# Kernel optimization log

Hardware: AMD Instinct MI355X
Metric: run time of the kernel (lower is better)

## Reference

```python
import jax, jax.numpy as jnp
import numpy as np
from jax import lax

B, T_ENC, T_DEC, H, L, F, NC, S = 1024, 128, 64, 128, 2, 16, 4, 8
X_DIM = 2
IN_DIM = X_DIM + F          # encoder GRU input_size = 18
H_ENC = 2 * H               # encoder hidden = 256 (mean/logvar)
H_DEC = H + NC              # decoder hidden = 132 (concat_cond_ts=False)


def _gru_params(key, in_dim, hid):
    k1, k2, k3, k4 = jax.random.split(key, 4)
    s = 1.0 / np.sqrt(hid)
    u = lambda k, shp: jax.random.uniform(k, shp, minval=-s, maxval=s, dtype=jnp.float32)
    return u(k1, (3 * hid, in_dim)), u(k2, (3 * hid, hid)), u(k3, (3 * hid,)), u(k4, (3 * hid,))


def gru_cell(x, h, Wih, Whh, bih, bhh):
    # torch GRU cell: r,z,n gate ordering
    gi = x @ Wih.T + bih
    gh = h @ Whh.T + bhh
    hd = h.shape[-1]
    ir, iz, inn = gi[:, :hd], gi[:, hd:2 * hd], gi[:, 2 * hd:]
    hr, hz, hn = gh[:, :hd], gh[:, hd:2 * hd], gh[:, 2 * hd:]
    r = jax.nn.sigmoid(ir + hr)
    zg = jax.nn.sigmoid(iz + hz)
    n = jnp.tanh(inn + r * hn)
    return (1.0 - zg) * n + zg * h


def setup_inputs() -> dict:
    key = jax.random.key(0)
    ks = jax.random.split(key, 12)
    x = jax.random.normal(ks[0], (B, T_ENC, X_DIM), dtype=jnp.float32)
    features = jax.random.normal(ks[1], (B, T_ENC + T_DEC, F), dtype=jnp.float32)
    lengths = jax.random.randint(ks[2], (B,), T_ENC // 2, T_ENC + 1)
    mask = (jnp.arange(T_ENC)[None, :] < lengths[:, None]).astype(jnp.int32)
    eps = jax.random.normal(ks[3], (S, L, B, H), dtype=jnp.float32)
    enc0 = _gru_params(ks[4], IN_DIM, H_ENC)
    enc1 = _gru_params(ks[5], H_ENC, H_ENC)
    dec0 = _gru_params(ks[6], 2, H_DEC)
    dec1 = _gru_params(ks[7], H_DEC, H_DEC)
    sm = 1.0 / np.sqrt(H)
    W1 = jax.random.uniform(ks[8], (H // 2, H), minval=-sm, maxval=sm, dtype=jnp.float32)
    b1 = jax.random.uniform(ks[9], (H // 2,), minval=-sm, maxval=sm, dtype=jnp.float32)
    s2 = 1.0 / np.sqrt(H // 2)
    W2 = jax.random.uniform(ks[10], (2, H // 2), minval=-s2, maxval=s2, dtype=jnp.float32)
    b2 = jax.random.uniform(ks[11], (2,), minval=-s2, maxval=s2, dtype=jnp.float32)
    return dict(
        x=x, features=features, mask=mask, eps=eps,
        nsteps_encode=T_ENC, nsteps_decode=T_DEC, n_elbo_samp=S,
        enc_Wih0=enc0[0], enc_Whh0=enc0[1], enc_bih0=enc0[2], enc_bhh0=enc0[3],
        enc_Wih1=enc1[0], enc_Whh1=enc1[1], enc_bih1=enc1[2], enc_bhh1=enc1[3],
        dec_Wih0=dec0[0], dec_Whh0=dec0[1], dec_bih0=dec0[2], dec_bhh0=dec0[3],
        dec_Wih1=dec1[0], dec_Whh1=dec1[1], dec_bih1=dec1[2], dec_bhh1=dec1[3],
        W1=W1, b1=b1, W2=W2, b2=b2,
    )


def reference(x, features, mask, eps, nsteps_encode, nsteps_decode, n_elbo_samp,
              enc_Wih0, enc_Whh0, enc_bih0, enc_bhh0,
              enc_Wih1, enc_Whh1, enc_bih1, enc_bhh1,
              dec_Wih0, dec_Whh0, dec_bih0, dec_bhh0,
              dec_Wih1, dec_Whh1, dec_bih1, dec_bhh1,
              W1, b1, W2, b2):
    n_hidden = W1.shape[1]
    batch = x.shape[0]
    enc_input = jnp.concatenate([x, features[:, :nsteps_encode, :]], axis=-1)
    m = mask.astype(bool)

    def mlp(h):
        return jax.nn.softplus(jax.nn.relu(h @ W1.T + b1) @ W2.T + b2)

    # --- encoder: 2-layer GRU with pack_padded semantics (freeze h / zero out past length) ---
    def enc_step(h, xm):
        xt, mt = xm
        h0n = gru_cell(xt, h[0], enc_Wih0, enc_Whh0, enc_bih0, enc_bhh0)
        h0n = jnp.where(mt[:, None], h0n, h[0])
        h1n = gru_cell(h0n, h[1], enc_Wih1, enc_Whh1, enc_bih1, enc_bhh1)
        h1n = jnp.where(mt[:, None], h1n, h[1])
        out = jnp.where(mt[:, None], h1n, 0.0)
        return jnp.stack([h0n, h1n]), out

    h_init = jnp.zeros((2, batch, enc_Whh0.shape[1]), dtype=x.dtype)
    hT, outs = lax.scan(enc_step, h_init, (enc_input.transpose(1, 0, 2), m.T))
    enc_out = outs.transpose(1, 0, 2)                 # [B, T_enc, 2H]
    enc_pred = mlp(enc_out[..., :n_hidden])           # [B, T_enc, 2]
    z_mean = hT[:, :, :n_hidden]                      # [L, B, H]
    z_logvar = hT[:, :, n_hidden:]

    last = enc_pred[:, -1, :]                         # [B, 2]
    feat_cond = features[:, nsteps_encode, :4]        # cond_inds = [0,1,2,3]

    # --- decoder: sequential single-step GRU, h0 = cat(z, cond feats) ---
    def decode_one(e):
        z = e * jnp.exp(0.5 * z_logvar) + z_mean      # [L, B, H]
        fc = jnp.broadcast_to(feat_cond[None], (z.shape[0],) + feat_cond.shape)
        h0 = jnp.concatenate([z, fc], axis=-1)        # [L, B, H+NC]
        def step(carry, _):
            inp, h = carry
            d0 = gru_cell(inp, h[0], dec_Wih0, dec_Whh0, dec_bih0, dec_bhh0)
            d1 = gru_cell(d0, h[1], dec_Wih1, dec_Whh1, dec_bih1, dec_bhh1)
            out = mlp(d1[:, :n_hidden])
            return (out, jnp.stack([d0, d1])), out
        _, outs_d = lax.scan(step, (last, h0), None, length=nsteps_decode - 1)
        return jnp.concatenate([last[None], outs_d], axis=0)   # [T_dec, B, 2]

    dec = jax.vmap(decode_one)(eps)                   # [S, T_dec, B, 2]
    dec_preds = dec.transpose(0, 2, 1, 3)             # [S, B, T_dec, 2]
    enc_stack = jnp.broadcast_to(enc_pred[None, :, :-1, :],
                                 (n_elbo_samp, batch, enc_pred.shape[1] - 1, 2))
    return enc_stack, dec_preds
```

## Files before the change

kernel.cpp:

```cpp
#include <hip/hip_runtime.h>
#include <hip/hip_bf16.h>
#include <math.h>

typedef __hip_bfloat16 bf16;
typedef short v8s __attribute__((ext_vector_type(8)));
typedef float v4f __attribute__((ext_vector_type(4)));

#define NB   1024
#define NT   128
#define NH   128
#define HE   256
#define HD   132
#define HDP  160
#define HDS  164
#define GDP  144
#define NS   8
#define KX   32
#define RG   16
#define NRG  64

namespace wsoff {
constexpr size_t al(size_t x){ return (x + 255) & ~size_t(255); }
constexpr size_t FLAG  = 0;
constexpr size_t CNT   = 256;
constexpr size_t XS    = al(CNT + 192*64);
constexpr size_t MASKT = al(XS    + (size_t)NT*NB*KX*2);
constexpr size_t WIH0  = al(MASKT + (size_t)NT*NB*4);
constexpr size_t WHH0  = al(WIH0  + 768*32*2);
constexpr size_t WIH1  = al(WHH0  + 768*256*2);
constexpr size_t WHH1  = al(WIH1  + 768*256*2);
constexpr size_t BIH0  = al(WHH1  + 768*256*2);
constexpr size_t BHH0  = al(BIH0  + 768*4);
constexpr size_t BIH1  = al(BHH0  + 768*4);
constexpr size_t BHH1  = al(BIH1  + 768*4);
constexpr size_t WDHH0 = al(BHH1  + 768*4);
constexpr size_t WDIH1 = al(WDHH0 + 432*HDP*2);
constexpr size_t WDHH1 = al(WDIH1 + 432*HDP*2);
constexpr size_t WDIH0F= al(WDHH1 + 432*HDP*2);
constexpr size_t BDIH0 = al(WDIH0F+ 792*4);
constexpr size_t BDHH0 = al(BDIH0 + 396*4);
constexpr size_t BDIH1 = al(BDHH0 + 396*4);
constexpr size_t BDHH1 = al(BDIH1 + 396*4);
constexpr size_t W1B   = al(BDHH1 + 396*4);
constexpr size_t B1F   = al(W1B   + 64*128*2);
constexpr size_t W2F   = al(B1F   + 64*4);
constexpr size_t B2F   = al(W2F   + 128*4);
constexpr size_t H0F0  = al(B2F   + 2*4);
constexpr size_t H1F0  = al(H0F0  + (size_t)NB*HE*4);
constexpr size_t RING0 = al(H1F0  + (size_t)NB*HE*4);
constexpr size_t RING1 = al(RING0 + (size_t)NRG*4*RG*256*2);
constexpr size_t ENCP  = al(RING1 + (size_t)128*2*RG*128*2);
}

__device__ __forceinline__ float ld_any(const void* p, size_t i, int isbf){
  return isbf ? __bfloat162float(((const bf16*)p)[i]) : ((const float*)p)[i];
}
__device__ __forceinline__ void st_out(void* out, size_t i, float v, int isbf){
  if (isbf) ((bf16*)out)[i] = __float2bfloat16(v); else ((float*)out)[i] = v;
}
__device__ __forceinline__ float sigm(float x){ return 1.0f/(1.0f + __expf(-x)); }
__device__ __forceinline__ float tanh_f(float x){
  float t = __expf(2.0f*x); return 1.0f - 2.0f/(t+1.0f);
}
__device__ __forceinline__ float softplusf(float x){ return x>20.f ? x : log1pf(__expf(x)); }
__device__ __forceinline__ v4f mfma16(v8s a, v8s b, v4f c){
  return __builtin_amdgcn_mfma_f32_16x16x32_bf16(a,b,c,0,0,0);
}
__device__ __forceinline__ v8s fragld(const bf16* base, size_t elem_off){
  return *reinterpret_cast<const v8s*>(base + elem_off);
}
__device__ __forceinline__ v8s ldsfrag(const short* sm, int unit, int lane){
  return *reinterpret_cast<const v8s*>(sm + (unit<<9) + (lane<<3));
}
__device__ __forceinline__ v8s lds_frag8(const short* p){
  union { long long l[2]; v8s s; } r;
  r.l[0] = *(const long long*)(p);
  r.l[1] = *(const long long*)(p + 4);
  return r.s;
}
__device__ __forceinline__ short bf16bits(float v){
  bf16 h = __float2bfloat16(v); short s; __builtin_memcpy(&s,&h,2); return s;
}
__device__ __forceinline__ float uasf(unsigned u){ float f; __builtin_memcpy(&f,&u,4); return f; }
__device__ __forceinline__ v8s ldg_coh16(const bf16* p){
  union { unsigned long long u[2]; v8s s; } r;
  const unsigned long long* q = (const unsigned long long*)p;
  r.u[0] = __hip_atomic_load(q+0, __ATOMIC_RELAXED, __HIP_MEMORY_SCOPE_AGENT);
  r.u[1] = __hip_atomic_load(q+1, __ATOMIC_RELAXED, __HIP_MEMORY_SCOPE_AGENT);
  return r.s;
}
__device__ __forceinline__ void stg_coh_pair(bf16* base_even, int lr, float v){
  bf16 h = __float2bfloat16(v);
  unsigned vv; { unsigned short b; __builtin_memcpy(&b, &h, 2); vv = b; }
  unsigned ov = (unsigned)__shfl_xor((int)vv, 1, 64);
  if (!(lr & 1))
    __hip_atomic_store((unsigned*)base_even, vv | (ov<<16), __ATOMIC_RELAXED, __HIP_MEMORY_SCOPE_AGENT);
}
__device__ __forceinline__ float*  f32p(char* ws, size_t off){ return (float*)(ws+off); }
__device__ __forceinline__ bf16*   bfp (char* ws, size_t off){ return (bf16*)(ws+off); }

__device__ __forceinline__ int* cntp(char* ws, int idx){
  return (int*)(ws + wsoff::CNT + (size_t)idx*64);
}
__device__ __forceinline__ void pollge(int* f, int v){
  while (__hip_atomic_load(f, __ATOMIC_RELAXED, __HIP_MEMORY_SCOPE_AGENT) < v)
    __builtin_amdgcn_s_sleep(1);
}
__device__ __forceinline__ void cntset(int* f, int v){
  __hip_atomic_store(f, v, __ATOMIC_RELAXED, __HIP_MEMORY_SCOPE_AGENT);
}

__global__ void k_detect(char* ws, const void* eps){
  const unsigned short* p = (const unsigned short*)eps;
  int lane = threadIdx.x;
  unsigned short u = p[2*lane];
  int e = (u>>7)&0xFF;
  bool pl = (e>=118 && e<=130);
  unsigned long long m = __ballot(pl);
  if (lane==0) *(int*)(ws+wsoff::FLAG) = (__popcll(m) >= 32) ? 1 : 0;
}

__global__ void k_stage_xs(char* ws, const void* x, const void* feat){
  int isbf = *(const int*)(ws+wsoff::FLAG);
  size_t i = (size_t)blockIdx.x*blockDim.x + threadIdx.x;
  if (i >= (size_t)NT*NB*KX) return;
  int c = i % KX; size_t q = i / KX; int b = q % NB; int t = q / NB;
  float v = 0.f;
  if (c < 2)        v = ld_any(x,    ((size_t)b*NT + t)*2 + c, isbf);
  else if (c < 18)  v = ld_any(feat, ((size_t)b*192 + t)*16 + (c-2), isbf);
  ((bf16*)(ws+wsoff::XS))[i] = __float2bfloat16(v);
}
__global__ void k_stage_maskT(char* ws, const int* mask){
  size_t i = (size_t)blockIdx.x*blockDim.x + threadIdx.x;
  if (i >= (size_t)NT*NB) return;
  int b = i % NB, t = i / NB;
  ((int*)(ws+wsoff::MASKT))[i] = mask[(size_t)b*NT + t];
}
__global__ void k_stage_pad(char* ws, const void* src, size_t dstoff, int R, int SC, int DC){
  int isbf = *(const int*)(ws+wsoff::FLAG);
  size_t i = (size_t)blockIdx.x*blockDim.x + threadIdx.x;
  if (i >= (size_t)R*DC) return;
  int r = i / DC, c = i % DC;
  float v = (c < SC) ? ld_any(src, (size_t)r*SC + c, isbf) : 0.f;
  ((bf16*)(ws+dstoff))[i] = __float2bfloat16(v);
}
__global__ void k_stage_dec(char* ws, const void* src, size_t dstoff){
  int isbf = *(const int*)(ws+wsoff::FLAG);
  size_t i = (size_t)blockIdx.x*blockDim.x + threadIdx.x;
  if (i >= (size_t)432*HDP) return;
  int R = i / HDP, c = i % HDP;
  int g = R / GDP, ii = R % GDP;
  float v = (ii < HD && c < HD) ? ld_any(src, ((size_t)(g*HD+ii))*HD + c, isbf) : 0.f;
  ((bf16*)(ws+dstoff))[i] = __float2bfloat16(v);
}
struct SmallSegs { const void* src[12]; int dstoff[12]; int n[12]; };
__global__ void k_stage_small(char* ws, SmallSegs segs){
  int isbf = *(const int*)(ws+wsoff::FLAG);
  int s = blockIdx.x;
  float* dst = (float*)(ws + (size_t)segs.dstoff[s]);
  for (int i = threadIdx.x; i < segs.n[s]; i += blockDim.x)
    dst[i] = ld_any(segs.src[s], i, isbf);
}

#define ENC_LDS 156928
__global__ __attribute__((amdgpu_flat_work_group_size(512,512), amdgpu_waves_per_eu(1)))
void k_encoder(char* ws){
  extern __shared__ __align__(16) char smem[];
  const int bid = blockIdx.x, tid = threadIdx.x;
  const int lane = tid & 63, w = tid >> 6, lr = lane & 15, q = lane >> 4;
  const int* maskT = (const int*)(ws + wsoff::MASKT);

  if (bid < NRG){
    constexpr int NL0 = 18;
    constexpr int NR0 = 54 - NL0;
    const int rb = bid, rowbase = rb*RG;
    short* wlds = (short*)smem;
    short* abuf = (short*)(smem + 8*NL0*1024);
    int* cL0 = cntp(ws, rb);
    int* cXa = cntp(ws, NRG + rb*2);
    int* cXb = cntp(ws, NRG + rb*2 + 1);
    const short* WH = (const short*)(ws + wsoff::WHH0);
    const short* WI = (const short*)(ws + wsoff::WIH0);
    for (int idx = tid; idx < 8*NL0*512; idx += 512){
      int slot = idx >> 9, le = idx & 511, ln = le >> 3, j = le & 7, lrr = ln & 15, qq = ln >> 4;
      int w2 = slot / NL0, i = slot % NL0;
      int kb = i % 9, t2 = i / 9, g = t2 % 3, cs = t2 / 3;
      int row = g*HE + w2*32 + cs*16 + lrr;
      wlds[idx] = (kb < 8) ? WH[(size_t)row*256 + kb*32 + qq*8 + j]
                           : WI[(size_t)row*32  + qq*8 + j];
    }
    for (int idx = tid; idx < RG*296; idx += 512) abuf[idx] = 0;
    v8s wreg[NR0];
    #pragma unroll
    for (int i = NL0; i < 54; ++i){
      int kb = i % 9, t2 = i / 9, g = t2 % 3, cs = t2 / 3;
      int row = g*HE + w*32 + cs*16 + lr;
      wreg[i-NL0] = (kb < 8) ? fragld(bfp(ws,wsoff::WHH0), (size_t)row*256 + kb*32 + q*8)
                             : fragld(bfp(ws,wsoff::WIH0), (size_t)row*32 + q*8);
    }
    const float* bih = f32p(ws,wsoff::BIH0);
    const float* bhh = f32p(ws,wsoff::BHH0);
    float birv[2], bizv[2], binv[2], bhnv[2];
    #pragma unroll
    for (int cs=0;cs<2;cs++){
      int d = w*32 + cs*16 + lr;
      birv[cs]=bih[d]+bhh[d]; bizv[cs]=bih[HE+d]+bhh[HE+d];
      binv[cs]=bih[2*HE+d];   bhnv[cs]=bhh[2*HE+d];
    }
    float h0a[2][4] = {};
    float* hTf = f32p(ws, wsoff::H0F0);
    bf16* ring0 = bfp(ws, wsoff::RING0) + (size_t)rb*4*RG*256;
    const bf16* Xs = bfp(ws,wsoff::XS);
    __syncthreads();
    for (int t = 0; t < 128; ++t){
      if (tid == 0 && t >= 4){
        pollge(cXa, t-3); pollge(cXb, t-3);
      }
      __syncthreads();
      if (tid < 64){
        int row = tid >> 2, ck = tid & 3;
        v8s xv = fragld(Xs, ((size_t)t*NB + rowbase + row)*KX + ck*8);
        *(v8s*)(abuf + row*296 + 256 + ck*8) = xv;
      }
      __syncthreads();
      v4f accr[2], accz[2], accxn[2], acchn[2];
      #pragma unroll
      for (int cs=0;cs<2;cs++){
        accr[cs]=(v4f){0,0,0,0}; accz[cs]=(v4f){0,0,0,0};
        accxn[cs]=(v4f){0,0,0,0}; acchn[cs]=(v4f){0,0,0,0};
      }
      #pragma unroll
      for (int kb=0;kb<9;kb++){
        v8s af = lds_frag8(abuf + lr*296 + kb*32 + q*8);
        #pragma unroll
        for (int cs=0;cs<2;cs++)
          #pragma unroll
          for (int g=0;g<3;g++){
            int i = (cs*3+g)*9 + kb;
            v8s b = (i < NL0) ? ldsfrag(wlds, w*NL0 + i, lane) : wreg[i-NL0];
            v4f* A = (g==0)?&accr[cs]:(g==1)?&accz[cs]:((kb<8)?&acchn[cs]:&accxn[cs]);
            *A = mfma16(af, b, *A);
          }
      }
      int mk[4];
      #pragma unroll
      for (int rr=0;rr<4;rr++) mk[rr] = maskT[(size_t)t*NB + rowbase + q*4 + rr];
      __syncthreads();
      bf16* slot = ring0 + (size_t)(t&3)*RG*256;
      #pragma unroll
      for (int cs=0;cs<2;cs++){
        int d = w*32 + cs*16 + lr;
        #pragma unroll
        for (int rr=0;rr<4;rr++){
          int row = q*4 + rr;
          float rg = sigm(accr[cs][rr] + birv[cs]);
          float zg = sigm(accz[cs][rr] + bizv[cs]);
          float nn = tanh_f(accxn[cs][rr] + binv[cs] + rg*(acchn[cs][rr]+bhnv[cs]));
          float hv = (1.f-zg)*nn + zg*h0a[cs][rr];
          float h2 = mk[rr] ? hv : h0a[cs][rr];
          h0a[cs][rr] = h2;
          abuf[row*296 + d] = bf16bits(h2);
          stg_coh_pair(slot + ((size_t)row*256 + (d & ~1)), lr, h2);
          if (t == 127) hTf[(size_t)(rowbase+row)*HE + d] = h2;
        }
      }
      __syncthreads();
      if (tid == 0) cntset(cL0, t+1);
    }
  } else {
    constexpr int NL1 = 15;
    constexpr int NR1 = 48 - NL1;
    const int id = bid - NRG, rb = id >> 1, ch = id & 1;
    const int rowbase = rb*RG;
    short* wlds = (short*)smem;
    short* abuf = (short*)(smem + 8*NL1*1024);
    short* w1s  = (short*)(smem + 8*NL1*1024 + RG*520*2);
    int* cL0 = cntp(ws, rb);
    int* cXo = cntp(ws, NRG + rb*2 + ch);
    int* cXp = cntp(ws, NRG + rb*2 + (ch^1));
    const short* WX = (const short*)(ws + wsoff::WIH1);
    const short* WHs= (const short*)(ws + wsoff::WHH1);
    for (int idx = tid; idx < 8*NL1*512; idx += 512){
      int slot = idx >> 9, le = idx & 511, ln = le >> 3, j = le & 7, lrr = ln & 15, qq = ln >> 4;
      int w2 = slot / NL1, i = slot % NL1;
      int kb = i & 15, g = i >> 4;
      int row = g*HE + ch*128 + w2*16 + lrr;
      wlds[idx] = (kb < 8) ? WX [(size_t)row*256 + kb*32 + qq*8 + j]
                           : WHs[(size_t)row*256 + (kb-8)*32 + qq*8 + j];
    }
    if (ch == 0){
      const short* W1s = (const short*)(ws + wsoff::W1B);
      for (int idx = tid; idx < 16*512; idx += 512){
        int u = idx >> 9, le = idx & 511, ln = le >> 3, j = le & 7, lrr = ln & 15, qq = ln >> 4;
        int c = u >> 2, kb = u & 3;
        w1s[idx] = W1s[(size_t)(c*16 + lrr)*NH + kb*32 + qq*8 + j];
      }
    }
    for (int idx = tid; idx < RG*520; idx += 512) abuf[idx] = 0;
    v8s wreg[NR1];
    #pragma unroll
    for (int i = NL1; i < 48; ++i){
      int kb = i & 15, g = i >> 4;
      int row = g*HE + ch*128 + w*16 + lr;
      wreg[i-NL1] = (kb < 8) ? fragld(bfp(ws,wsoff::WIH1), (size_t)row*256 + kb*32 + q*8)
                             : fragld(bfp(ws,wsoff::WHH1), (size_t)row*256 + (kb-8)*32 + q*8);
    }
    const float* bih = f32p(ws,wsoff::BIH1);
    const float* bhh = f32p(ws,wsoff::BHH1);
    const int d = ch*128 + w*16 + lr;
    const float birv=bih[d]+bhh[d], bizv=bih[HE+d]+bhh[HE+d];
    const float binv=bih[2*HE+d],   bhnv=bhh[2*HE+d];
    float h1a[4] = {};
    float b1v[4], w20[4], w21[4];
    #pragma unroll
    for (int c=0;c<4;c++){
      int col=c*16+lr;
      b1v[c]=f32p(ws,wsoff::B1F)[col];
      w20[c]=f32p(ws,wsoff::W2F)[col]; w21[c]=f32p(ws,wsoff::W2F)[64+col];
    }
    const float b20 = f32p(ws,wsoff::B2F)[0], b21 = f32p(ws,wsoff::B2F)[1];
    float* hTf = f32p(ws, wsoff::H1F0);
    const bf16* ring0 = bfp(ws, wsoff::RING0) + (size_t)rb*4*RG*256;
    bf16* ring1o       = bfp(ws, wsoff::RING1) + (size_t)id*2*RG*128;
    const bf16* ring1p = bfp(ws, wsoff::RING1) + (size_t)(id^1)*2*RG*128;
    float* encp = f32p(ws,wsoff::ENCP);
    __syncthreads();
    for (int s = 0; s < 128; ++s){
      if (tid == 0){
        pollge(cL0, s+1);
        if (s >= 1) pollge(cXp, s);
      }
      __syncthreads();
      {
        const bf16* hs = ring0 + (size_t)(s&3)*RG*256;
        int row = tid >> 5, ck = tid & 31;
        v8s v = ldg_coh16(hs + (size_t)row*256 + ck*8);
        *(v8s*)(abuf + row*520 + ck*8) = v;
      }
      if (s >= 1 && tid < 256){
        const bf16* hp = ring1p + (size_t)((s-1)&1)*RG*128;
        int row = tid >> 4, ck = tid & 15;
        v8s v = ldg_coh16(hp + (size_t)row*128 + ck*8);
        *(v8s*)(abuf + row*520 + 256 + (ch^1)*128 + ck*8) = v;
      }
      __syncthreads();
      v4f accr=(v4f){0,0,0,0}, accz=(v4f){0,0,0,0};
      v4f accxn=(v4f){0,0,0,0}, acchn=(v4f){0,0,0,0};
      #pragma unroll
      for (int kb=0;kb<16;kb++){
        v8s af = lds_frag8(abuf + lr*520 + kb*32 + q*8);
        #pragma unroll
        for (int g=0;g<3;g++){
          int i = g*16 + kb;
          v8s b = (i < NL1) ? ldsfrag(wlds, w*NL1 + i, lane) : wreg[i-NL1];
          v4f* A = (g==0)?&accr:(g==1)?&accz:((kb<8)?&accxn:&acchn);
          *A = mfma16(af, b, *A);
        }
      }
      int mk[4];
      #pragma unroll
      for (int rr=0;rr<4;rr++) mk[rr] = maskT[(size_t)s*NB + rowbase + q*4 + rr];
      __syncthreads();
      bf16* slot = ring1o + (size_t)(s&1)*RG*128;
      #pragma unroll
      for (int rr=0;rr<4;rr++){
        int row = q*4 + rr;
        float rg = sigm(accr[rr] + birv);
        float zg = sigm(accz[rr] + bizv);
        float nn = tanh_f(accxn[rr] + binv + rg*(acchn[rr]+bhnv));
        float hv = (1.f-zg)*nn + zg*h1a[rr];
        float h2 = mk[rr] ? hv : h1a[rr];
        h1a[rr] = h2;
        int ch_col = w*16 + lr;
        abuf[row*520 + 256 + ch*128 + ch_col] = bf16bits(h2);
        stg_coh_pair(slot + ((size_t)row*128 + (ch_col & ~1)), lr, h2);
        if (s == 127) hTf[(size_t)(rowbase+row)*HE + d] = h2;
      }
      __syncthreads();
      if (tid == 0) cntset(cXo, s+1);
      if (ch == 0 && w == 0){
        int vl = maskT[(size_t)s*NB + rowbase + lr];
        v4f acc[4];
        #pragma unroll
        for (int c=0;c<4;c++) acc[c]=(v4f){0,0,0,0};
        #pragma unroll
        for (int kb=0;kb<4;kb++){
          v8s af = vl ? lds_frag8(abuf + lr*520 + 256 + kb*32 + q*8)
                      : (v8s){0,0,0,0,0,0,0,0};
          #pragma unroll
          for (int c=0;c<4;c++) acc[c] = mfma16(af, ldsfrag(w1s, c*4+kb, lane), acc[c]);
        }
        float* outp = encp + (size_t)s*NB*2;
        #pragma unroll
        for (int rr=0;rr<4;rr++){
          float p0=0.f, p1=0.f;
          #pragma unroll
          for (int c=0;c<4;c++){
            float hv = acc[c][rr] + b1v[c]; hv = hv>0.f ? hv : 0.f;
            p0 += hv*w20[c]; p1 += hv*w21[c];
          }
          #pragma unroll
          for (int m=1;m<16;m<<=1){ p0 += __shfl_xor(p0,m,64); p1 += __shfl_xor(p1,m,64); }
          if (lr == 0){
            int grow = rowbase + q*4 + rr;
            outp[(size_t)grow*2]   = softplusf(p0+b20);
            outp[(size_t)grow*2+1] = softplusf(p1+b21);
          }
        }
      }
    }
  }
}

#define DEC_LDS 163296
__global__ __attribute__((amdgpu_flat_work_group_size(512,512), amdgpu_waves_per_eu(1)))
void k_decoder(char* ws, const void* eps, const void* feat, void* out){
  extern __shared__ __align__(16) char dsm[];
  short* s_h0b = (short*)dsm;
  short* s_h1b = s_h0b + 32*HDS;
  float* s_inp = (float*)(dsm + 20992);
  float* s_red = (float*)(dsm + 21248);
  short* s_wh  = (short*)(dsm + 21760);
  short* s_ct  = (short*)(dsm + 144640);
  float* s_tail= (float*)(dsm + 160000);
  float* s_th  = (float*)(dsm + 162048);
  float* s_tt0 = (float*)(dsm + 163072);
  float* s_tt1 = (float*)(dsm + 163232);

  const int isbf = *(const int*)(ws+wsoff::FLAG);
  const int tid = threadIdx.x;
  const int lane = tid & 63, w = tid >> 6, lr = lane & 15, q = lane >> 4;
  const int rowbase = blockIdx.x*32;
  constexpr size_t N0v = (size_t)NS*NB*127*2;

  const bf16* W0g  = bfp(ws,wsoff::WDHH0);
  const bf16* WX1g = bfp(ws,wsoff::WDIH1);

  for (int i = tid; i < 2*32*HDS; i += 512) s_h0b[i] = 0;
  {
    const short* src = (const short*)(ws + wsoff::WDHH1);
    for (int idx = tid; idx < 120*512; idx += 512){
      int u = idx >> 9, le = idx & 511, ln = le >> 3, e = le & 7, lrr = ln & 15, qq = ln >> 4;
      int kb = u % 5, t2 = u / 5, cc = t2 & 7, g = t2 >> 3;
      s_wh[idx] = src[(size_t)(g*GDP + cc*16 + lrr)*HDP + kb*32 + qq*8 + e];
    }
  }
  {
    const short* g0 = (const short*)(ws + wsoff::WDHH0);
    const short* gx = (const short*)(ws + wsoff::WDIH1);
    const short* gh = (const short*)(ws + wsoff::WDHH1);
    for (int idx = tid; idx < 5*512; idx += 512){
      int kb = idx >> 9, le = idx & 511, l = le >> 3, j = le & 7, lrr = l & 15, qq = l >> 4;
      short v0 = 0, vx = 0, vh = 0;
      if (lrr < 12){
        int g = lrr >> 2, cc = lrr & 3;
        size_t so = (size_t)(g*GDP + 128 + cc)*HDP + kb*32 + qq*8 + j;
        v0 = g0[so]; vx = gx[so];
        if (lrr < 8) vh = gh[so];
      } else {
        int cc = lrr & 3;
        size_t so = (size_t)(2*GDP + 128 + cc)*HDP + kb*32 + qq*8 + j;
        vh = gh[so];
      }
      s_ct[idx]          = v0;
      s_ct[5*512 + idx]  = vx;
      s_ct[10*512 + idx] = vh;
    }
  }
  if (tid < 4){
    const float* wih = f32p(ws,wsoff::WDIH0F);
    const float* bi0 = f32p(ws,wsoff::BDIH0); const float* bh0 = f32p(ws,wsoff::BDHH0);
    const float* bi1 = f32p(ws,wsoff::BDIH1); const float* bh1 = f32p(ws,wsoff::BDHH1);
    int dd = 128 + tid;
    float* T = s_tt0 + tid*10;
    T[0]=wih[(0*HD+dd)*2]; T[1]=wih[(0*HD+dd)*2+1];
    T[2]=wih[(1*HD+dd)*2]; T[3]=wih[(1*HD+dd)*2+1];
    T[4]=wih[(2*HD+dd)*2]; T[5]=wih[(2*HD+dd)*2+1];
    T[6]=bi0[dd]+bh0[dd]; T[7]=bi0[HD+dd]+bh0[HD+dd]; T[8]=bi0[2*HD+dd]; T[9]=bh0[2*HD+dd];
    float* T1 = s_tt1 + tid*4;
    T1[0]=bi1[dd]+bh1[dd]; T1[1]=bi1[HD+dd]+bh1[HD+dd]; T1[2]=bi1[2*HD+dd]; T1[3]=bh1[2*HD+dd];
  }
  if (tid < 64){
    int r0 = tid >> 1, c = tid & 1;
    int b = (rowbase + r0) & 1023;
    float v = f32p(ws,wsoff::ENCP)[((size_t)127*NB + b)*2 + c];
    s_inp[tid] = v;
    st_out(out, N0v + ((size_t)(rowbase+r0)*64)*2 + c, v, isbf);
  }
  __syncthreads();

  const int d = w*16 + lr;
  float e0a[10], e1a[4];
  {
    const float* wih = f32p(ws,wsoff::WDIH0F);
    const float* bi0 = f32p(ws,wsoff::BDIH0); const float* bh0 = f32p(ws,wsoff::BDHH0);
    const float* bi1 = f32p(ws,wsoff::BDIH1); const float* bh1 = f32p(ws,wsoff::BDHH1);
    e0a[0]=wih[(0*HD+d)*2]; e0a[1]=wih[(0*HD+d)*2+1];
    e0a[2]=wih[(1*HD+d)*2]; e0a[3]=wih[(1*HD+d)*2+1];
    e0a[4]=wih[(2*HD+d)*2]; e0a[5]=wih[(2*HD+d)*2+1];
    e0a[6]=bi0[d]+bh0[d]; e0a[7]=bi0[HD+d]+bh0[HD+d]; e0a[8]=bi0[2*HD+d]; e0a[9]=bh0[2*HD+d];
    e1a[0]=bi1[d]+bh1[d]; e1a[1]=bi1[HD+d]+bh1[HD+d]; e1a[2]=bi1[2*HD+d]; e1a[3]=bh1[2*HD+d];
  }
  float h0a[2][4], h1a[2][4];
  {
    const float* h0T = f32p(ws,wsoff::H0F0);
    const float* h1T = f32p(ws,wsoff::H1F0);
    #pragma unroll
    for (int m=0;m<2;m++)
      #pragma unroll
      for (int r=0;r<4;r++){
        int row = m*16 + q*4 + r, grow = rowbase + row;
        int s = grow >> 10, b = grow & 1023;
        float e0 = ld_any(eps, ((size_t)(s*2+0)*NB + b)*NH + d, isbf);
        float e1 = ld_any(eps, ((size_t)(s*2+1)*NB + b)*NH + d, isbf);
        float v0 = e0*__expf(0.5f*h0T[(size_t)b*HE + NH + d]) + h0T[(size_t)b*HE + d];
        float v1 = e1*__expf(0.5f*h1T[(size_t)b*HE + NH + d]) + h1T[(size_t)b*HE + d];
        h0a[m][r] = v0; h1a[m][r] = v1;
        s_h0b[row*HDS + d] = bf16bits(v0);
        s_h1b[row*HDS + d] = bf16bits(v1);
      }
  }
  if (tid < 128){
    int c4 = tid >> 5, row = tid & 31;
    int b = (rowbase + row) & 1023;
    float fc = ld_any(feat, (size_t)b*3072 + 2048 + c4, isbf);
    s_th[row*4 + c4] = fc;
    s_th[128 + row*4 + c4] = fc;
    s_h0b[row*HDS + 128 + c4] = bf16bits(fc);
    s_h1b[row*HDS + 128 + c4] = bf16bits(fc);
  }
  v8s w0f[3][5], wxf[3][5];
  #pragma unroll
  for (int g=0;g<3;g++)
    #pragma unroll
    for (int kb=0;kb<5;kb++){
      size_t off = (size_t)(g*GDP + w*16 + lr)*HDP + kb*32 + q*8;
      w0f[g][kb] = fragld(W0g, off);
      wxf[g][kb] = fragld(WX1g, off);
    }
  const float b20 = f32p(ws,wsoff::B2F)[0], b21 = f32p(ws,wsoff::B2F)[1];
  __syncthreads();

  for (int k = 0; k < 63; ++k){
    v4f p1[3][2]; v4f pt[2];
    #pragma unroll
    for (int g=0;g<3;g++){ p1[g][0]=(v4f){0,0,0,0}; p1[g][1]=(v4f){0,0,0,0}; }
    pt[0]=(v4f){0,0,0,0}; pt[1]=(v4f){0,0,0,0};
    #pragma unroll
    for (int m=0;m<2;m++)
      #pragma unroll
      for (int kb=0;kb<5;kb++){
        v8s A = lds_frag8(s_h0b + (m*16+lr)*HDS + kb*32 + q*8);
        #pragma unroll
        for (int g=0;g<3;g++) p1[g][m] = mfma16(A, w0f[g][kb], p1[g][m]);
        if (w == 7) pt[m] = mfma16(A, ldsfrag(s_ct, kb, lane), pt[m]);
      }
    if (w == 7 && lr < 12){
      #pragma unroll
      for (int m=0;m<2;m++)
        #pragma unroll
        for (int r=0;r<4;r++)
          s_tail[lr*32 + m*16 + q*4 + r] = pt[m][r];
    }
    __syncthreads();
    #pragma unroll
    for (int m=0;m<2;m++)
      #pragma unroll
      for (int r=0;r<4;r++){
        int row = m*16 + q*4 + r;
        float i0 = s_inp[row*2], i1 = s_inp[row*2+1];
        float rr = sigm(i0*e0a[0]+i1*e0a[1] + p1[0][m][r] + e0a[6]);
        float zz = sigm(i0*e0a[2]+i1*e0a[3] + p1[1][m][r] + e0a[7]);
        float nn = tanh_f(i0*e0a[4]+i1*e0a[5] + e0a[8] + rr*(p1[2][m][r] + e0a[9]));
        float h = (1.f-zz)*nn + zz*h0a[m][r];
        h0a[m][r] = h;
        s_h0b[row*HDS + d] = bf16bits(h);
      }
    if (tid < 128){
      int c4 = tid >> 5, row = tid & 31;
      float ar = s_tail[(0*4+c4)*32+row], az = s_tail[(1*4+c4)*32+row], an = s_tail[(2*4+c4)*32+row];
      const float* T = s_tt0 + c4*10;
      float i0 = s_inp[row*2], i1 = s_inp[row*2+1];
      float rr = sigm(i0*T[0]+i1*T[1] + ar + T[6]);
      float zz = sigm(i0*T[2]+i1*T[3] + az + T[7]);
      float nn = tanh_f(i0*T[4]+i1*T[5] + T[8] + rr*(an + T[9]));
      float ho = s_th[row*4 + c4];
      float h = (1.f-zz)*nn + zz*ho;
      s_th[row*4 + c4] = h;
      s_h0b[row*HDS + 128 + c4] = bf16bits(h);
    }
    __syncthreads();
    v4f p2[4][2]; v4f pt2[2];
    #pragma unroll
    for (int g=0;g<4;g++){ p2[g][0]=(v4f){0,0,0,0}; p2[g][1]=(v4f){0,0,0,0}; }
    pt2[0]=(v4f){0,0,0,0}; pt2[1]=(v4f){0,0,0,0};
    #pragma unroll
    for (int m=0;m<2;m++)
      #pragma unroll
      for (int kb=0;kb<5;kb++){
        v8s ax = lds_frag8(s_h0b + (m*16+lr)*HDS + kb*32 + q*8);
        v8s ah = lds_frag8(s_h1b + (m*16+lr)*HDS + kb*32 + q*8);
        #pragma unroll
        for (int g=0;g<3;g++){
          int aix = (g==2) ? 2 : g, aih = (g==2) ? 3 : g;
          p2[aix][m] = mfma16(ax, wxf[g][kb], p2[aix][m]);
          p2[aih][m] = mfma16(ah, ldsfrag(s_wh, (g*8+w)*5 + kb, lane), p2[aih][m]);
        }
        if (w == 7){
          pt2[m] = mfma16(ax, ldsfrag(s_ct, 5 + kb, lane), pt2[m]);
          pt2[m] = mfma16(ah, ldsfrag(s_ct, 10 + kb, lane), pt2[m]);
        }
      }
    if (w == 7){
      #pragma unroll
      for (int m=0;m<2;m++)
        #pragma unroll
        for (int r=0;r<4;r++)
          s_tail[lr*32 + m*16 + q*4 + r] = pt2[m][r];
    }
    __syncthreads();
    #pragma unroll
    for (int m=0;m<2;m++)
      #pragma unroll
      for (int r=0;r<4;r++){
        int row = m*16 + q*4 + r;
        float rr = sigm(p2[0][m][r] + e1a[0]);
        float zz = sigm(p2[1][m][r] + e1a[1]);
        float nn = tanh_f(p2[2][m][r] + e1a[2] + rr*(p2[3][m][r] + e1a[3]));
        float h = (1.f-zz)*nn + zz*h1a[m][r];
        h1a[m][r] = h;
        s_h1b[row*HDS + d] = bf16bits(h);
      }
    if (tid < 128){
      int c4 = tid >> 5, row = tid & 31;
      float tr = s_tail[(0*4+c4)*32+row], tz = s_tail[(1*4+c4)*32+row];
      float txn = s_tail[(2*4+c4)*32+row], thn = s_tail[(3*4+c4)*32+row];
      const float* T1 = s_tt1 + c4*4;
      float rr = sigm(tr + T1[0]);
      float zz = sigm(tz + T1[1]);
      float nn = tanh_f(txn + T1[2] + rr*(thn + T1[3]));
      float ho = s_th[128 + row*4 + c4];
      float h = (1.f-zz)*nn + zz*ho;
      s_th[128 + row*4 + c4] = h;
      s_h1b[row*HDS + 128 + c4] = bf16bits(h);
    }
    __syncthreads();
    if (w == 5 || w == 6){
      const int tb = (w-5)*2;
      const bf16* W1g = bfp(ws,wsoff::W1B);
      v8s w1a[2][4];
      float b1vv[2], w20vv[2], w21vv[2];
      #pragma unroll
      for (int ct=0;ct<2;ct++){
        #pragma unroll
        for (int kb=0;kb<4;kb++)
          w1a[ct][kb] = fragld(W1g, (size_t)((tb+ct)*16+lr)*NH + kb*32 + q*8);
        b1vv[ct]  = f32p(ws,wsoff::B1F)[(tb+ct)*16+lr];
        w20vv[ct] = f32p(ws,wsoff::W2F)[(tb+ct)*16+lr];
        w21vv[ct] = f32p(ws,wsoff::W2F)[64+(tb+ct)*16+lr];
      }
      v4f a3[2][2];
      #pragma unroll
      for (int ct=0;ct<2;ct++){ a3[ct][0]=(v4f){0,0,0,0}; a3[ct][1]=(v4f){0,0,0,0}; }
      #pragma unroll
      for (int m=0;m<2;m++)
        #pragma unroll
        for (int kb=0;kb<4;kb++){
          v8s A = lds_frag8(s_h1b + (m*16+lr)*HDS + kb*32 + q*8);
          #pragma unroll
          for (int ct=0;ct<2;ct++) a3[ct][m] = mfma16(A, w1a[ct][kb], a3[ct][m]);
        }
      #pragma unroll
      for (int m=0;m<2;m++)
        #pragma unroll
        for (int r=0;r<4;r++){
          float p0 = 0.f, p1v = 0.f;
          #pragma unroll
          for (int ct=0;ct<2;ct++){
            float hv = a3[ct][m][r] + b1vv[ct]; hv = hv > 0.f ? hv : 0.f;
            p0 += hv*w20vv[ct]; p1v += hv*w21vv[ct];
          }
          #pragma unroll
          for (int mm=1;mm<16;mm<<=1){ p0 += __shfl_xor(p0,mm,64); p1v += __shfl_xor(p1v,mm,64); }
          if (lr == 0){
            int row = m*16 + q*4 + r;
            s_red[(w-5)*64 + row*2]   = p0;
            s_red[(w-5)*64 + row*2+1] = p1v;
          }
        }
    }
    __syncthreads();
    if (tid < 64){
      int row = tid >> 1, c = tid & 1;
      float p = s_red[row*2 + c] + s_red[64 + row*2 + c];
      float v = softplusf(p + (c ? b21 : b20));
      s_inp[tid] = v;
      st_out(out, N0v + ((size_t)(rowbase+row)*64 + (k+1))*2 + c, v, isbf);
    }
    __syncthreads();
  }
}

__global__ void k_assemble_enc(char* ws, void* out){
  int isbf = *(const int*)(ws+wsoff::FLAG);
  const float* encp = f32p(ws,wsoff::ENCP);
  constexpr size_t N0v = (size_t)NS*NB*127*2;
  for (size_t i = (size_t)blockIdx.x*blockDim.x + threadIdx.x; i < N0v;
       i += (size_t)gridDim.x*blockDim.x){
    int c = (int)(i & 1); size_t qq = i >> 1;
    int tt = (int)(qq % 127); size_t q2 = qq / 127; int b = (int)(q2 & 1023);
    st_out(out, i, encp[((size_t)tt*NB + b)*2 + c], isbf);
  }
}

extern "C" void kernel_launch(void* const* d_in, const int* in_sizes, int n_in,
                              void* d_out, int out_size, void* d_ws, size_t ws_size,
                              hipStream_t stream) {
  char* ws = (char*)d_ws;
  const int* mask = (const int*)d_in[2];
  auto gb = [](size_t n){ return dim3((unsigned)((n + 255)/256)); };

  hipMemsetAsync(ws+wsoff::CNT, 0, 192*64, stream);

  k_detect<<<1,64,0,stream>>>(ws, d_in[3]);

  k_stage_xs   <<<gb((size_t)NT*NB*KX),256,0,stream>>>(ws, d_in[0], d_in[1]);
  k_stage_maskT<<<gb((size_t)NT*NB),256,0,stream>>>(ws, mask);
  k_stage_pad<<<gb(768*32) ,256,0,stream>>>(ws, d_in[7],  wsoff::WIH0, 768, 18, 32);
  k_stage_pad<<<gb(768*256),256,0,stream>>>(ws, d_in[8],  wsoff::WHH0, 768, 256, 256);
  k_stage_pad<<<gb(768*256),256,0,stream>>>(ws, d_in[11], wsoff::WIH1, 768, 256, 256);
  k_stage_pad<<<gb(768*256),256,0,stream>>>(ws, d_in[12], wsoff::WHH1, 768, 256, 256);
  k_stage_pad<<<gb(64*128) ,256,0,stream>>>(ws, d_in[23], wsoff::W1B,  64, 128, 128);
  k_stage_dec<<<gb(432*HDP),256,0,stream>>>(ws, d_in[16], wsoff::WDHH0);
  k_stage_dec<<<gb(432*HDP),256,0,stream>>>(ws, d_in[19], wsoff::WDIH1);
  k_stage_dec<<<gb(432*HDP),256,0,stream>>>(ws, d_in[20], wsoff::WDHH1);

  SmallSegs ss;
  const void* srcs[12] = {d_in[9],d_in[10],d_in[13],d_in[14],d_in[15],
                          d_in[17],d_in[18],d_in[21],d_in[22],
                          d_in[24],d_in[25],d_in[26]};
  const size_t offs[12] = {wsoff::BIH0,wsoff::BHH0,wsoff::BIH1,wsoff::BHH1,wsoff::WDIH0F,
                           wsoff::BDIH0,wsoff::BDHH0,wsoff::BDIH1,wsoff::BDHH1,
                           wsoff::B1F,wsoff::W2F,wsoff::B2F};
  const int ns[12] = {768,768,768,768,792,396,396,396,396,64,128,2};
  for (int i=0;i<12;i++){ ss.src[i]=srcs[i]; ss.dstoff[i]=(int)offs[i]; ss.n[i]=ns[i]; }
  k_stage_small<<<12,256,0,stream>>>(ws, ss);

  hipFuncSetAttribute(reinterpret_cast<const void*>(k_encoder),
                      hipFuncAttributeMaxDynamicSharedMemorySize, ENC_LDS);
  hipFuncSetAttribute(reinterpret_cast<const void*>(k_decoder),
                      hipFuncAttributeMaxDynamicSharedMemorySize, DEC_LDS);

  k_encoder<<<192,512,ENC_LDS,stream>>>(ws);
  k_decoder<<<256,512,DEC_LDS,stream>>>(ws, d_in[3], d_in[1], d_out);
  k_assemble_enc<<<2048,256,0,stream>>>(ws, d_out);
}
```

Before: 1.946 ms.

## Keep decoder tail gates in wave 7 via shuffles and overlap next-step layer-0 MFMA

The decoder's 4-column tail gate results are no longer staged through shared memory for 128 threads to read. Wave 7 now computes those gates itself using cross-lane shuffles of its MFMA accumulators. The layer-0 recurrent MFMA for the next step moves to just after the MLP block, before the barrier, which removes one __syncthreads per step and overlaps that matmul with the output reduction. In exchange, wave 7 does serial tail work with lane divergence (only 4 of 16 lanes active), and the reordering depends on s_inp being written after run_p1 reads only s_h0b.

```diff
diff --git a/kernel.cpp b/kernel.cpp
--- a/kernel.cpp
+++ b/kernel.cpp
@@ -422,7 +422,6 @@
   float* s_red = (float*)(dsm + 21248);
   short* s_wh  = (short*)(dsm + 21760);
   short* s_ct  = (short*)(dsm + 144640);
-  float* s_tail= (float*)(dsm + 160000);
   float* s_th  = (float*)(dsm + 162048);
   float* s_tt0 = (float*)(dsm + 163072);
   float* s_tt1 = (float*)(dsm + 163232);
@@ -521,13 +520,13 @@
       }
   }
   if (tid < 128){
-    int c4 = tid >> 5, row = tid & 31;
+    int c4i = tid >> 5, row = tid & 31;
     int b = (rowbase + row) & 1023;
-    float fc = ld_any(feat, (size_t)b*3072 + 2048 + c4, isbf);
-    s_th[row*4 + c4] = fc;
-    s_th[128 + row*4 + c4] = fc;
-    s_h0b[row*HDS + 128 + c4] = bf16bits(fc);
-    s_h1b[row*HDS + 128 + c4] = bf16bits(fc);
+    float fc = ld_any(feat, (size_t)b*3072 + 2048 + c4i, isbf);
+    s_th[row*4 + c4i] = fc;
+    s_th[128 + row*4 + c4i] = fc;
+    s_h0b[row*HDS + 128 + c4i] = bf16bits(fc);
+    s_h1b[row*HDS + 128 + c4i] = bf16bits(fc);
   }
   v8s w0f[3][5], wxf[3][5];
   #pragma unroll
@@ -541,8 +540,9 @@
   const float b20 = f32p(ws,wsoff::B2F)[0], b21 = f32p(ws,wsoff::B2F)[1];
   __syncthreads();
 
-  for (int k = 0; k < 63; ++k){
-    v4f p1[3][2]; v4f pt[2];
+  const int tc4 = lane & 3;
+  v4f p1[3][2]; v4f pt[2];
+  auto run_p1 = [&](){
     #pragma unroll
     for (int g=0;g<3;g++){ p1[g][0]=(v4f){0,0,0,0}; p1[g][1]=(v4f){0,0,0,0}; }
     pt[0]=(v4f){0,0,0,0}; pt[1]=(v4f){0,0,0,0};
@@ -555,13 +555,10 @@
         for (int g=0;g<3;g++) p1[g][m] = mfma16(A, w0f[g][kb], p1[g][m]);
         if (w == 7) pt[m] = mfma16(A, ldsfrag(s_ct, kb, lane), pt[m]);
       }
-    if (w == 7 && lr < 12){
-      #pragma unroll
-      for (int m=0;m<2;m++)
-        #pragma unroll
-        for (int r=0;r<4;r++)
-          s_tail[lr*32 + m*16 + q*4 + r] = pt[m][r];
-    }
+  };
+  run_p1();
+
+  for (int k = 0; k < 63; ++k){
     __syncthreads();
     #pragma unroll
     for (int m=0;m<2;m++)
@@ -576,18 +573,27 @@
         h0a[m][r] = h;
         s_h0b[row*HDS + d] = bf16bits(h);
       }
-    if (tid < 128){
-      int c4 = tid >> 5, row = tid & 31;
-      float ar = s_tail[(0*4+c4)*32+row], az = s_tail[(1*4+c4)*32+row], an = s_tail[(2*4+c4)*32+row];
-      const float* T = s_tt0 + c4*10;
-      float i0 = s_inp[row*2], i1 = s_inp[row*2+1];
-      float rr = sigm(i0*T[0]+i1*T[1] + ar + T[6]);
-      float zz = sigm(i0*T[2]+i1*T[3] + az + T[7]);
-      float nn = tanh_f(i0*T[4]+i1*T[5] + T[8] + rr*(an + T[9]));
-      float ho = s_th[row*4 + c4];
-      float h = (1.f-zz)*nn + zz*ho;
-      s_th[row*4 + c4] = h;
-      s_h0b[row*HDS + 128 + c4] = bf16bits(h);
+    if (w == 7){
+      #pragma unroll
+      for (int m=0;m<2;m++)
+        #pragma unroll
+        for (int r=0;r<4;r++){
+          float ar = __shfl(pt[m][r], (lane & 48) | tc4, 64);
+          float az = __shfl(pt[m][r], (lane & 48) | (4+tc4), 64);
+          float an = __shfl(pt[m][r], (lane & 48) | (8+tc4), 64);
+          if (lr < 4){
+            int row = m*16 + q*4 + r;
+            const float* T = s_tt0 + tc4*10;
+            float i0 = s_inp[row*2], i1 = s_inp[row*2+1];
+            float rg = sigm(i0*T[0]+i1*T[1] + ar + T[6]);
+            float zg = sigm(i0*T[2]+i1*T[3] + az + T[7]);
+            float nn = tanh_f(i0*T[4]+i1*T[5] + T[8] + rg*(an + T[9]));
+            float ho = s_th[row*4 + tc4];
+            float h = (1.f-zg)*nn + zg*ho;
+            s_th[row*4 + tc4] = h;
+            s_h0b[row*HDS + 128 + tc4] = bf16bits(h);
+          }
+        }
     }
     __syncthreads();
     v4f p2[4][2]; v4f pt2[2];
@@ -611,13 +617,6 @@
           pt2[m] = mfma16(ah, ldsfrag(s_ct, 10 + kb, lane), pt2[m]);
         }
       }
-    if (w == 7){
-      #pragma unroll
-      for (int m=0;m<2;m++)
-        #pragma unroll
-        for (int r=0;r<4;r++)
-          s_tail[lr*32 + m*16 + q*4 + r] = pt2[m][r];
-    }
     __syncthreads();
     #pragma unroll
     for (int m=0;m<2;m++)
@@ -631,18 +630,27 @@
         h1a[m][r] = h;
         s_h1b[row*HDS + d] = bf16bits(h);
       }
-    if (tid < 128){
-      int c4 = tid >> 5, row = tid & 31;
-      float tr = s_tail[(0*4+c4)*32+row], tz = s_tail[(1*4+c4)*32+row];
-      float txn = s_tail[(2*4+c4)*32+row], thn = s_tail[(3*4+c4)*32+row];
-      const float* T1 = s_tt1 + c4*4;
-      float rr = sigm(tr + T1[0]);
-      float zz = sigm(tz + T1[1]);
-      float nn = tanh_f(txn + T1[2] + rr*(thn + T1[3]));
-      float ho = s_th[128 + row*4 + c4];
-      float h = (1.f-zz)*nn + zz*ho;
-      s_th[128 + row*4 + c4] = h;
-      s_h1b[row*HDS + 128 + c4] = bf16bits(h);
+    if (w == 7){
+      #pragma unroll
+      for (int m=0;m<2;m++)
+        #pragma unroll
+        for (int r=0;r<4;r++){
+          float tr  = __shfl(pt2[m][r], (lane & 48) | tc4, 64);
+          float tz  = __shfl(pt2[m][r], (lane & 48) | (4+tc4), 64);
+          float txn = __shfl(pt2[m][r], (lane & 48) | (8+tc4), 64);
+          float thn = __shfl(pt2[m][r], (lane & 48) | (12+tc4), 64);
+          if (lr < 4){
+            int row = m*16 + q*4 + r;
+            const float* T1 = s_tt1 + tc4*4;
+            float rg = sigm(tr + T1[0]);
+            float zg = sigm(tz + T1[1]);
+            float nn = tanh_f(txn + T1[2] + rg*(thn + T1[3]));
+            float ho = s_th[128 + row*4 + tc4];
+            float h = (1.f-zg)*nn + zg*ho;
+            s_th[128 + row*4 + tc4] = h;
+            s_h1b[row*HDS + 128 + tc4] = bf16bits(h);
+          }
+        }
     }
     __syncthreads();
     if (w == 5 || w == 6){
@@ -689,6 +697,7 @@
           }
         }
     }
+    run_p1();
     __syncthreads();
     if (tid < 64){
       int row = tid >> 1, c = tid & 1;
@@ -697,7 +706,6 @@
       s_inp[tid] = v;
       st_out(out, N0v + ((size_t)(rowbase+row)*64 + (k+1))*2 + c, v, isbf);
     }
-    __syncthreads();
   }
 }
 
```

New measurement: 2.285 ms. 17.4% more time.
